# Optimization experiments

Hardware: AMD Instinct MI355X
Metric: run time of the kernel (lower is better)

## Reference

```python
import jax, jax.numpy as jnp
import numpy as np


def setup_inputs() -> dict:
    key = jax.random.key(0)
    k1, k2 = jax.random.split(key)
    B, H, W, E = 8, 32, 32, 256   # latent grid (NHWC layout, as in vector_quantize)
    N_E = 16384                   # codebook size
    x = jax.random.normal(k1, (B, H, W, E), dtype=jnp.float32)
    codebook = jax.random.normal(k2, (N_E, E), dtype=jnp.float32)
    return {"x": x, "codebook": codebook}


def reference(x, codebook):
    # d[b,h,w,k] = ||x[b,h,w] - codebook[k]||^2 (expanded form, as in source)
    x_sq = jnp.sum(x * x, axis=-1, keepdims=True)            # [B,H,W,1]
    cb_sq = jnp.sum(codebook * codebook, axis=1)              # [N_E]
    cross = jnp.einsum('bhwe,ke->bhwk', x, codebook)          # [B,H,W,N_E]
    d = x_sq + cb_sq - 2.0 * cross
    indices = jnp.argmin(d, axis=-1)                          # [B,H,W]
    x_q = jnp.take(codebook, indices, axis=0)                 # one-hot @ codebook == row gather
    # straight-through / ReplaceGrad: forward value is x_q, gradient flows to x
    return x + jax.lax.stop_gradient(x_q - x)
```

## Files before the change

kernel.cpp:

```cpp
#include <hip/hip_runtime.h>
#include <stdint.h>

#define M_PIX 8192
#define N_CB  16384
#define KD    256

typedef float f32x4 __attribute__((ext_vector_type(4)));
typedef long long ll2 __attribute__((ext_vector_type(2)));
typedef unsigned long long ull;

#define OFF_CF8  (0ULL)
#define OFF_XF8  (4ULL << 20)
#define OFF_CBSQ (6ULL << 20)
#define OFF_SLOT (7ULL << 20)
#define WS_REQ   (15ULL << 20)

__device__ __forceinline__ unsigned int fkey(float s) {
  unsigned int f = __float_as_uint(s);
  return f ^ ((unsigned int)(((int)f) >> 31) | 0x80000000u);
}
__device__ __forceinline__ unsigned char f2e4m3(float v) {
  float av = fminf(fabsf(v), 448.0f);
  const unsigned s = (__float_as_uint(v) >> 24) & 0x80u;
  unsigned m;
  if (av >= 0.015625f) {
    unsigned u = __float_as_uint(av);
    u += 0x7FFFFu + ((u >> 20) & 1u);
    m = (((u >> 23) - 120u) << 3) | ((u >> 20) & 7u);
  } else {
    m = (unsigned)(int)rintf(av * 512.0f);
  }
  return (unsigned char)(s | m);
}
__device__ __forceinline__ void gl_lds16(const unsigned char* g, char* l) {
  __builtin_amdgcn_global_load_lds(
      (const __attribute__((address_space(1))) unsigned int*)(const void*)g,
      (__attribute__((address_space(3))) unsigned int*)(void*)l,
      16, 0, 0);
}
__device__ __forceinline__ void ins2f(float k, float& v1, float& v2) {
  v2 = fminf(v2, fmaxf(v1, k));
  v1 = fminf(v1, k);
}

__global__ __launch_bounds__(256) void prep_kernel(
    const float* __restrict__ x, const float* __restrict__ cb,
    unsigned char* __restrict__ Cf8, unsigned char* __restrict__ Xf8,
    float* __restrict__ cbsq) {
  const int wid = threadIdx.x >> 6, lane = threadIdx.x & 63;
  const int row = blockIdx.x * 4 + wid;
  const bool isCb = (row < N_CB);
  const int rowL = isCb ? row : row - N_CB;
  const float* src = (isCb ? cb : x) + (size_t)rowL * KD;
  const float4 v = ((const float4*)src)[lane];
  const int k0 = lane * 4;
  const int p0 = (k0 & 0x87) | ((k0 & 0x18) << 2) | ((k0 >> 2) & 0x18);
  uchar4 pk;
  pk.x = f2e4m3(v.x); pk.y = f2e4m3(v.y); pk.z = f2e4m3(v.z); pk.w = f2e4m3(v.w);
  *(uchar4*)(void*)((isCb ? Cf8 : Xf8) + (size_t)rowL * KD + p0) = pk;
  if (isCb) {
    float ss = v.x*v.x + v.y*v.y + v.z*v.z + v.w*v.w;
    #pragma unroll
    for (int off = 32; off > 0; off >>= 1) ss += __shfl_xor(ss, off);
    if (lane == 0) cbsq[rowL] = ss;
  }
}


__global__ __launch_bounds__(256, 4) void gemm_top2_kernel(
    const unsigned char* __restrict__ Xf8, const unsigned char* __restrict__ Cf8,
    const float* __restrict__ cbsq, float2* __restrict__ slots) {
  __shared__ __align__(16) char smem[36864];
  char* A_s = smem;
  char* B_s = smem + 16384;
  float* v1p = (float*)smem;
  float* v2p = (float*)(smem + 18432);

  const int tid = threadIdx.x;
  const int wid = tid >> 6, lane = tid & 63;
  const int wy = wid >> 1, wx = wid & 1;
  const int q = lane >> 4, c = lane & 15;

  const int bx = blockIdx.x & 7, bg = blockIdx.x >> 3;
  const int mt = bg >> 4;
  const int nt = bx * 16 + (bg & 15);
  const int m0 = mt * 128, n0 = nt * 128;

  int abase[4], bbase[4];
  #pragma unroll
  for (int i = 0; i < 4; i++) {
    abase[i] = (wy * 64 + i * 16 + c) * 128 + q * 32;
    bbase[i] = (wx * 64 + i * 16 + c) * 128 + q * 32;
  }

  const f32x4 zf = {0.f, 0.f, 0.f, 0.f};
  f32x4 acc[4][4];
  #pragma unroll
  for (int i = 0; i < 4; i++)
    #pragma unroll
    for (int j = 0; j < 4; j++) acc[i][j] = zf;

  #pragma unroll
  for (int hk = 0; hk < 2; hk++) {
    if (hk) __syncthreads();
    #pragma unroll
    for (int j = 0; j < 4; j++) {
      const int chunk = j * 4 + wid;
      const int row = chunk * 8 + (lane >> 3);
      const int gb = (lane & 7) * 16 + hk * 128;
      gl_lds16(Xf8 + (size_t)(m0 + row) * KD + gb, A_s + chunk * 1024);
      gl_lds16(Cf8 + (size_t)(n0 + row) * KD + gb, B_s + chunk * 1024);
    }
    __syncthreads();
    #pragma unroll
    for (int kp = 0; kp < 2; kp++) {
      ll2 bfr[4];
      #pragma unroll
      for (int ni = 0; ni < 4; ni++)
        bfr[ni] = *(const ll2*)(const void*)(B_s + bbase[ni] + kp * 16);
      #pragma unroll
      for (int mi = 0; mi < 4; mi++) {
        const ll2 af = *(const ll2*)(const void*)(A_s + abase[mi] + kp * 16);
        #pragma unroll
        for (int ni = 0; ni < 4; ni++) {
          acc[mi][ni] = __builtin_amdgcn_mfma_f32_16x16x32_fp8_fp8(af.x, bfr[ni].x, acc[mi][ni], 0, 0, 0);
          acc[mi][ni] = __builtin_amdgcn_mfma_f32_16x16x32_fp8_fp8(af.y, bfr[ni].y, acc[mi][ni], 0, 0, 0);
        }
      }
    }
  }
  __syncthreads();

  float cs[4]; unsigned colp[4];
  #pragma unroll
  for (int ni = 0; ni < 4; ni++) {
    colp[ni] = wx * 64 + ni * 16 + c;
    cs[ni] = cbsq[n0 + colp[ni]];
  }
  const float FINF = __uint_as_float(0x7F800000u);

  #pragma unroll
  for (int mi = 0; mi < 4; mi++) {
    #pragma unroll
    for (int r = 0; r < 4; r++) {
      float v1 = FINF, v2 = FINF;
      #pragma unroll
      for (int ni = 0; ni < 4; ni++) {
        const float s = fmaf(-2.f, acc[mi][ni][r], cs[ni]);
        ins2f(__uint_as_float((__float_as_uint(s) & 0xFFFFFF80u) | colp[ni]),
              v1, v2);
      }
      const int row = wy * 64 + mi * 16 + q * 4 + r;
      const int slot = wx * 16 + c;
      v1p[row * 36 + slot] = v1;
      v2p[row * 36 + slot] = v2;
    }
  }
  __syncthreads();

  {
    const int srow = tid >> 1, half = tid & 1;
    float v1 = FINF, v2 = FINF;
    #pragma unroll
    for (int jj = 0; jj < 2; jj++) {
      const float4 a = *(const float4*)(const void*)(v1p + srow * 36 + half * 16 + jj * 8);
      const float4 a2 = *(const float4*)(const void*)(v1p + srow * 36 + half * 16 + jj * 8 + 4);
      const float4 b = *(const float4*)(const void*)(v2p + srow * 36 + half * 16 + jj * 8);
      const float4 b2 = *(const float4*)(const void*)(v2p + srow * 36 + half * 16 + jj * 8 + 4);
      ins2f(a.x, v1, v2);  ins2f(a.y, v1, v2);
      ins2f(a.z, v1, v2);  ins2f(a.w, v1, v2);
      ins2f(a2.x, v1, v2); ins2f(a2.y, v1, v2);
      ins2f(a2.z, v1, v2); ins2f(a2.w, v1, v2);
      ins2f(b.x, v1, v2);  ins2f(b.y, v1, v2);
      ins2f(b.z, v1, v2);  ins2f(b.w, v1, v2);
      ins2f(b2.x, v1, v2); ins2f(b2.y, v1, v2);
      ins2f(b2.z, v1, v2); ins2f(b2.w, v1, v2);
    }
    const float b1 = __shfl_xor(v1, 1), b2 = __shfl_xor(v2, 1);
    const float hi = fmaxf(v1, b1);
    v1 = fminf(v1, b1);
    v2 = fminf(fminf(v2, b2), hi);
    if (!half)
      slots[(size_t)nt * M_PIX + m0 + srow] = make_float2(v1, v2);
  }
}

__global__ __launch_bounds__(256) void reduce_rescore_gather(
    const float* __restrict__ x, const float* __restrict__ cb,
    const float* __restrict__ cbsq, const float2* __restrict__ slots,
    float* __restrict__ out) {
  const int wid = threadIdx.x >> 6, lane = threadIdx.x & 63;
  const int pixel = blockIdx.x * 4 + wid;

  const float2 sA = slots[(size_t)lane * M_PIX + pixel];
  const float2 sB = slots[(size_t)(64 + lane) * M_PIX + pixel];
  const float sc[4] = {sA.x, sA.y, sB.x, sB.y};
  float mn = fminf(fminf(sc[0], sc[1]), fminf(sc[2], sc[3]));
  #pragma unroll
  for (int off = 1; off < 64; off <<= 1) mn = fminf(mn, __shfl_xor(mn, off));
  const float thr = mn + 10.0f;

  const float4 xv = ((const float4*)x)[(size_t)pixel * 64 + lane];
  ull best = ~0ULL;
  #pragma unroll
  for (int j = 0; j < 4; j++) {
    ull mask = __ballot(sc[j] < thr);
    while (mask) {
      const int src = (int)__ffsll((long long)mask) - 1;
      mask &= mask - 1;
      const float val = __shfl(sc[j], src);
      const unsigned ij = (unsigned)(((j >> 1) * 64 + src) * 128) +
                          (__float_as_uint(val) & 127u);
      const float4 cv = ((const float4*)cb)[(size_t)ij * 64 + lane];
      float d = xv.x*cv.x + xv.y*cv.y + xv.z*cv.z + xv.w*cv.w;
      #pragma unroll
      for (int off = 1; off < 64; off <<= 1) d += __shfl_xor(d, off);
      const float sv = fmaf(-2.f, d, cbsq[ij]);
      const ull k = ((ull)fkey(sv) << 32) | ij;
      best = k < best ? k : best;
    }
  }
  const unsigned w = (unsigned)best;
  ((float4*)out)[(size_t)pixel * 64 + lane] = ((const float4*)cb)[(size_t)w * 64 + lane];
}

__global__ __launch_bounds__(256) void fallback_kernel(
    const float* __restrict__ x, const float* __restrict__ cb,
    float* __restrict__ out) {
  __shared__ float xs[256];
  __shared__ unsigned long long keys[4];
  __shared__ int widx;
  const int p = blockIdx.x;
  const int tid = threadIdx.x, wid = tid >> 6, lane = tid & 63;
  xs[tid] = x[(size_t)p * KD + tid];
  __syncthreads();
  const float4 xv = ((const float4*)xs)[lane];
  float bestS = 3.4e38f; int bestI = 0;
  for (int k = wid; k < N_CB; k += 4) {
    const float4 cv = ((const float4*)cb)[(size_t)k * 64 + lane];
    float t = cv.x*(cv.x - 2.f*xv.x) + cv.y*(cv.y - 2.f*xv.y)
            + cv.z*(cv.z - 2.f*xv.z) + cv.w*(cv.w - 2.f*xv.w);
    #pragma unroll
    for (int off = 1; off < 64; off <<= 1) t += __shfl_xor(t, off);
    if (t < bestS) { bestS = t; bestI = k; }
  }
  if (lane == 0)
    keys[wid] = ((unsigned long long)fkey(bestS) << 32) | (unsigned int)bestI;
  __syncthreads();
  if (tid == 0) {
    unsigned long long m = keys[0];
    for (int i = 1; i < 4; i++) if (keys[i] < m) m = keys[i];
    widx = (int)(unsigned int)(m & 0xFFFFFFFFULL);
  }
  __syncthreads();
  out[(size_t)p * KD + tid] = cb[(size_t)widx * KD + tid];
}

extern "C" void kernel_launch(void* const* d_in, const int* in_sizes, int n_in,
                              void* d_out, int out_size, void* d_ws, size_t ws_size,
                              hipStream_t stream) {
  const float* x  = (const float*)d_in[0];
  const float* cb = (const float*)d_in[1];
  float* out = (float*)d_out;

  if (ws_size < WS_REQ) {
    fallback_kernel<<<M_PIX, 256, 0, stream>>>(x, cb, out);
    return;
  }

  char* ws = (char*)d_ws;
  unsigned char* Cf8 = (unsigned char*)(ws + OFF_CF8);
  unsigned char* Xf8 = (unsigned char*)(ws + OFF_XF8);
  float* cbsq        = (float*)(ws + OFF_CBSQ);
  float2* slots      = (float2*)(ws + OFF_SLOT);

  prep_kernel<<<(N_CB + M_PIX) / 4, 256, 0, stream>>>(x, cb, Cf8, Xf8, cbsq);
  gemm_top2_kernel<<<M_PIX, 256, 0, stream>>>(Xf8, Cf8, cbsq, slots);
  reduce_rescore_gather<<<M_PIX / 4, 256, 0, stream>>>(x, cb, cbsq, slots, out);
}
```

Baseline: 154.7 us.

## Swizzle GEMM LDS layout and batch rescore candidates per 64-pixel block

Applies an XOR swizzle to the fp8 LDS tile layout for both the global-to-LDS writes and the MFMA operand reads, to cut LDS bank conflicts in the GEMM. It also restructures the rescore kernel so each block handles 64 pixels. Candidates under the threshold are gathered into a shared list with atomics and rescored by all waves, replacing the per-pixel wave loop with serial ballot iteration. The candidate list is capped at 1536 entries, which could drop candidates when near-ties are dense.

```diff
diff --git a/kernel.cpp b/kernel.cpp
--- a/kernel.cpp
+++ b/kernel.cpp
@@ -89,8 +89,8 @@
   int abase[4], bbase[4];
   #pragma unroll
   for (int i = 0; i < 4; i++) {
-    abase[i] = (wy * 64 + i * 16 + c) * 128 + q * 32;
-    bbase[i] = (wx * 64 + i * 16 + c) * 128 + q * 32;
+    abase[i] = (wy * 64 + i * 16 + c) * 128 + (((2 * q) ^ (c & 7)) << 4);
+    bbase[i] = (wx * 64 + i * 16 + c) * 128 + (((2 * q) ^ (c & 7)) << 4);
   }
 
   const f32x4 zf = {0.f, 0.f, 0.f, 0.f};
@@ -99,6 +99,8 @@
   for (int i = 0; i < 4; i++)
     #pragma unroll
     for (int j = 0; j < 4; j++) acc[i][j] = zf;
+
+  const int sg = (lane & 7) ^ ((lane >> 3) & 7);
 
   #pragma unroll
   for (int hk = 0; hk < 2; hk++) {
@@ -107,7 +109,7 @@
     for (int j = 0; j < 4; j++) {
       const int chunk = j * 4 + wid;
       const int row = chunk * 8 + (lane >> 3);
-      const int gb = (lane & 7) * 16 + hk * 128;
+      const int gb = sg * 16 + hk * 128;
       gl_lds16(Xf8 + (size_t)(m0 + row) * KD + gb, A_s + chunk * 1024);
       gl_lds16(Cf8 + (size_t)(n0 + row) * KD + gb, B_s + chunk * 1024);
     }
@@ -117,10 +119,10 @@
       ll2 bfr[4];
       #pragma unroll
       for (int ni = 0; ni < 4; ni++)
-        bfr[ni] = *(const ll2*)(const void*)(B_s + bbase[ni] + kp * 16);
+        bfr[ni] = *(const ll2*)(const void*)(B_s + (bbase[ni] ^ (kp << 4)));
       #pragma unroll
       for (int mi = 0; mi < 4; mi++) {
-        const ll2 af = *(const ll2*)(const void*)(A_s + abase[mi] + kp * 16);
+        const ll2 af = *(const ll2*)(const void*)(A_s + (abase[mi] ^ (kp << 4)));
         #pragma unroll
         for (int ni = 0; ni < 4; ni++) {
           acc[mi][ni] = __builtin_amdgcn_mfma_f32_16x16x32_fp8_fp8(af.x, bfr[ni].x, acc[mi][ni], 0, 0, 0);
@@ -163,9 +165,9 @@
     float v1 = FINF, v2 = FINF;
     #pragma unroll
     for (int jj = 0; jj < 2; jj++) {
-      const float4 a = *(const float4*)(const void*)(v1p + srow * 36 + half * 16 + jj * 8);
+      const float4 a  = *(const float4*)(const void*)(v1p + srow * 36 + half * 16 + jj * 8);
       const float4 a2 = *(const float4*)(const void*)(v1p + srow * 36 + half * 16 + jj * 8 + 4);
-      const float4 b = *(const float4*)(const void*)(v2p + srow * 36 + half * 16 + jj * 8);
+      const float4 b  = *(const float4*)(const void*)(v2p + srow * 36 + half * 16 + jj * 8);
       const float4 b2 = *(const float4*)(const void*)(v2p + srow * 36 + half * 16 + jj * 8 + 4);
       ins2f(a.x, v1, v2);  ins2f(a.y, v1, v2);
       ins2f(a.z, v1, v2);  ins2f(a.w, v1, v2);
@@ -189,39 +191,80 @@
     const float* __restrict__ x, const float* __restrict__ cb,
     const float* __restrict__ cbsq, const float2* __restrict__ slots,
     float* __restrict__ out) {
-  const int wid = threadIdx.x >> 6, lane = threadIdx.x & 63;
-  const int pixel = blockIdx.x * 4 + wid;
-
-  const float2 sA = slots[(size_t)lane * M_PIX + pixel];
-  const float2 sB = slots[(size_t)(64 + lane) * M_PIX + pixel];
-  const float sc[4] = {sA.x, sA.y, sB.x, sB.y};
-  float mn = fminf(fminf(sc[0], sc[1]), fminf(sc[2], sc[3]));
-  #pragma unroll
-  for (int off = 1; off < 64; off <<= 1) mn = fminf(mn, __shfl_xor(mn, off));
-  const float thr = mn + 10.0f;
-
-  const float4 xv = ((const float4*)x)[(size_t)pixel * 64 + lane];
-  ull best = ~0ULL;
-  #pragma unroll
-  for (int j = 0; j < 4; j++) {
-    ull mask = __ballot(sc[j] < thr);
-    while (mask) {
-      const int src = (int)__ffsll((long long)mask) - 1;
-      mask &= mask - 1;
-      const float val = __shfl(sc[j], src);
-      const unsigned ij = (unsigned)(((j >> 1) * 64 + src) * 128) +
-                          (__float_as_uint(val) & 127u);
-      const float4 cv = ((const float4*)cb)[(size_t)ij * 64 + lane];
-      float d = xv.x*cv.x + xv.y*cv.y + xv.z*cv.z + xv.w*cv.w;
-      #pragma unroll
-      for (int off = 1; off < 64; off <<= 1) d += __shfl_xor(d, off);
+  __shared__ float pmin[64][4];
+  __shared__ ull wbest[64][4];
+  __shared__ unsigned cand[1536];
+  __shared__ int ncand;
+
+  const int tid = threadIdx.x;
+  const int wid = tid >> 6, lane = tid & 63;
+  const int P0 = blockIdx.x * 64;
+  const int pl = tid & 63;
+  const int tg = tid >> 6;
+
+  if (tid < 64) {
+    #pragma unroll
+    for (int w = 0; w < 4; w++) wbest[tid][w] = ~0ULL;
+  }
+  if (tid == 0) ncand = 0;
+
+  const float FINF = __uint_as_float(0x7F800000u);
+  float m = FINF;
+  for (int s = 0; s < 32; s++) {
+    const float2 v = slots[(size_t)(s * 4 + tg) * M_PIX + P0 + pl];
+    m = fminf(m, v.x);
+  }
+  pmin[pl][tg] = m;
+  __syncthreads();
+  const float thr = fminf(fminf(pmin[pl][0], pmin[pl][1]),
+                          fminf(pmin[pl][2], pmin[pl][3])) + 10.0f;
+
+  for (int s = 0; s < 32; s++) {
+    const int t = s * 4 + tg;
+    const float2 v = slots[(size_t)t * M_PIX + P0 + pl];
+    if (v.x < thr) {
+      const int i = atomicAdd(&ncand, 1);
+      if (i < 1536)
+        cand[i] = ((unsigned)pl << 14) | (unsigned)(t * 128 + (__float_as_uint(v.x) & 127u));
+    }
+    if (v.y < thr) {
+      const int i = atomicAdd(&ncand, 1);
+      if (i < 1536)
+        cand[i] = ((unsigned)pl << 14) | (unsigned)(t * 128 + (__float_as_uint(v.y) & 127u));
+    }
+  }
+  __syncthreads();
+
+  const int nc = min(ncand, 1536);
+  for (int ci = wid; ci < nc; ci += 4) {
+    const unsigned e = cand[ci];
+    const int p = (int)(e >> 14);
+    const unsigned ij = e & 0x3FFFu;
+    const float4 xv = ((const float4*)x)[(size_t)(P0 + p) * 64 + lane];
+    const float4 cv = ((const float4*)cb)[(size_t)ij * 64 + lane];
+    float d = xv.x*cv.x + xv.y*cv.y + xv.z*cv.z + xv.w*cv.w;
+    #pragma unroll
+    for (int off = 1; off < 64; off <<= 1) d += __shfl_xor(d, off);
+    if (lane == 0) {
       const float sv = fmaf(-2.f, d, cbsq[ij]);
       const ull k = ((ull)fkey(sv) << 32) | ij;
-      best = k < best ? k : best;
-    }
-  }
-  const unsigned w = (unsigned)best;
-  ((float4*)out)[(size_t)pixel * 64 + lane] = ((const float4*)cb)[(size_t)w * 64 + lane];
+      const ull cur = wbest[p][wid];
+      wbest[p][wid] = k < cur ? k : cur;
+    }
+  }
+  __syncthreads();
+
+  #pragma unroll
+  for (int r = 0; r < 16; r++) {
+    const int p = r * 4 + wid;
+    const ull b0 = wbest[p][0], b1 = wbest[p][1],
+              b2 = wbest[p][2], b3 = wbest[p][3];
+    ull b = b0 < b1 ? b0 : b1;
+    const ull b23 = b2 < b3 ? b2 : b3;
+    b = b < b23 ? b : b23;
+    const unsigned w = (unsigned)b;
+    ((float4*)out)[(size_t)(P0 + p) * 64 + lane] = ((const float4*)cb)[(size_t)w * 64 + lane];
+  }
 }
 
 __global__ __launch_bounds__(256) void fallback_kernel(
@@ -276,5 +319,5 @@
 
   prep_kernel<<<(N_CB + M_PIX) / 4, 256, 0, stream>>>(x, cb, Cf8, Xf8, cbsq);
   gemm_top2_kernel<<<M_PIX, 256, 0, stream>>>(Xf8, Cf8, cbsq, slots);
-  reduce_rescore_gather<<<M_PIX / 4, 256, 0, stream>>>(x, cb, cbsq, slots, out);
-}
+  reduce_rescore_gather<<<M_PIX / 64, 256, 0, stream>>>(x, cb, cbsq, slots, out);
+}
```

New measurement: 178.7 us. 1.16x slower.
